# Kernel optimization log

Measured on AMD Instinct MI355X. Metric: run time of the kernel, lower is better.

## Reference

```python
import jax, jax.numpy as jnp
import numpy as np

B, L, D = 1, 4096, 1024
H, HD = 16, 64

def setup_inputs() -> dict:
    key = jax.random.key(0)
    ks = jax.random.split(key, 5)
    scale = 1.0 / np.sqrt(D)
    return {
        "x": jax.random.normal(ks[0], (B, L, D), dtype=jnp.float32),
        "Wq": jax.random.normal(ks[1], (D, D), dtype=jnp.float32) * scale,
        "Wk": jax.random.normal(ks[2], (D, D), dtype=jnp.float32) * scale,
        "Wv": jax.random.normal(ks[3], (D, D), dtype=jnp.float32) * scale,
        "Wo": jax.random.normal(ks[4], (D, D), dtype=jnp.float32) * scale,
    }

def reference(x, Wq, Wk, Wv, Wo):
    Bc, Lc, _ = x.shape
    # torch Linear: y = x @ W.T
    q = (x @ Wq.T).reshape(Bc, Lc, H, HD).transpose(0, 2, 1, 3)  # [B,H,L,hd]
    k = (x @ Wk.T).reshape(Bc, Lc, H, HD).transpose(0, 2, 1, 3)
    v = (x @ Wv.T).reshape(Bc, Lc, H, HD).transpose(0, 2, 1, 3)
    scale = HD ** -0.5
    scores = jnp.einsum('bhqd,bhkd->bhqk', q, k) * scale  # [B,H,L,L]
    causal = jnp.tril(jnp.ones((Lc, Lc), dtype=bool))
    scores = jnp.where(causal, scores, -jnp.inf)
    attn = jax.nn.softmax(scores, axis=-1)
    out = jnp.einsum('bhqk,bhkd->bhqd', attn, v)
    out = out.transpose(0, 2, 1, 3).reshape(Bc, Lc, H * HD)
    return out @ Wo.T
```

## Files before the change

### kernel.cpp

```cpp
#include <hip/hip_runtime.h>
#include <hip/hip_bf16.h>
#include <stdint.h>

#define L_SEQ   4096
#define D_MODEL 1024
#define N_HEADS 16
#define HEAD_DIM 64

typedef uint16_t u16;
typedef __bf16 bf16x8 __attribute__((ext_vector_type(8)));
typedef short s16x4 __attribute__((ext_vector_type(4)));
typedef float floatx4 __attribute__((ext_vector_type(4)));

__device__ __forceinline__ floatx4 mfma32(bf16x8 a, bf16x8 b, floatx4 c) {
  return __builtin_amdgcn_mfma_f32_16x16x32_bf16(a, b, c, 0, 0, 0);
}

__device__ __forceinline__ float hw_exp2(float x) {
  return __builtin_amdgcn_exp2f(x);
}

__device__ __forceinline__ uint32_t fbits(float f) {
  union { float f; uint32_t u; } x; x.f = f; return x.u;
}

__device__ __forceinline__ uint32_t pack_bf16_trunc(float f1, float f0) {
  return __builtin_amdgcn_perm(fbits(f1), fbits(f0), 0x07060302u);
}

__device__ __forceinline__ void load16_lds(const u16* g, u16* l) {
  __builtin_amdgcn_global_load_lds(
      (const __attribute__((address_space(1))) void*)g,
      (__attribute__((address_space(3))) void*)l, 16, 0, 0);
}

__device__ __forceinline__ u16 f2bf(float f) {
  uint32_t u = fbits(f);
  uint32_t r = u + 0x7FFFu + ((u >> 16) & 1u);
  return (u16)(r >> 16);
}

#define Q_PRESCALE 0.18033688011112042f

__global__ __launch_bounds__(256) void cvt_kernel(
    const float* __restrict__ x,  const float* __restrict__ wq,
    const float* __restrict__ wk, const float* __restrict__ wv,
    const float* __restrict__ wo,
    u16* __restrict__ xb, u16* __restrict__ wqb, u16* __restrict__ wkb,
    u16* __restrict__ wvb, u16* __restrict__ wob) {
  const int z = blockIdx.z;
  const float* s; u16* d; int n;
  if (z == 0)      { s = x;  d = xb;  n = L_SEQ * D_MODEL; }
  else if (z == 1) { s = wq; d = wqb; n = D_MODEL * D_MODEL; }
  else if (z == 2) { s = wk; d = wkb; n = D_MODEL * D_MODEL; }
  else if (z == 3) { s = wv; d = wvb; n = D_MODEL * D_MODEL; }
  else             { s = wo; d = wob; n = D_MODEL * D_MODEL; }
  const int stride = gridDim.x * 256 * 4;
  for (int i = (blockIdx.x * 256 + threadIdx.x) * 4; i < n; i += stride) {
    float4 v = *(const float4*)(s + i);
    ushort4 o;
    o.x = f2bf(v.x); o.y = f2bf(v.y); o.z = f2bf(v.z); o.w = f2bf(v.w);
    *(ushort4*)(d + i) = o;
  }
}

__global__ __launch_bounds__(256) void qkv_gemm_kernel(
    const u16* __restrict__ X,
    const u16* __restrict__ Wq, const u16* __restrict__ Wk, const u16* __restrict__ Wv,
    u16* __restrict__ Qo, u16* __restrict__ Ko, u16* __restrict__ VTo) {
  constexpr int BK = 32, Kdim = D_MODEL, NIT = Kdim / BK;
  __shared__ __align__(16) u16 As[2][128 * BK];
  __shared__ __align__(16) u16 Bs[2][128 * BK];

  const int b = blockIdx.x;
  const int g = b & 7, i2 = b >> 3;
  const int z = i2 % 3, j = i2 / 3;
  const int x = (g & 3) * 8 + (j & 7);
  const int y = (g >> 2) * 4 + (j >> 3);

  const u16* __restrict__ A;
  const u16* __restrict__ B;
  int m0, n0;
  if (z < 2) { A = X; B = z ? Wk : Wq; m0 = x * 128; n0 = y * 128; }
  else       { A = Wv; B = X;          m0 = y * 128; n0 = x * 128; }

  const int tid = threadIdx.x;
  const int wave = tid >> 6, lane = tid & 63;
  const int wm = wave & 1, wn = wave >> 1;
  const int quad = lane >> 4, l15 = lane & 15;

  floatx4 acc[4][4] = {};

  const int cbase = wave * 128;
  const int c0 = cbase + lane, c1 = c0 + 64;
  const int r0 = c0 >> 2, cc0 = (c0 & 3) * 8;
  const int r1 = c1 >> 2, cc1 = (c1 & 3) * 8;

  auto stage = [&](int k0, int sel) {
    load16_lds(&A[(size_t)(m0 + r0) * Kdim + k0 + cc0], &As[sel][cbase * 8]);
    load16_lds(&A[(size_t)(m0 + r1) * Kdim + k0 + cc1], &As[sel][(cbase + 64) * 8]);
    load16_lds(&B[(size_t)(n0 + r0) * Kdim + k0 + cc0], &Bs[sel][cbase * 8]);
    load16_lds(&B[(size_t)(n0 + r1) * Kdim + k0 + cc1], &Bs[sel][(cbase + 64) * 8]);
  };

  stage(0, 0);
  for (int kk = 0; kk < NIT; ++kk) {
    __syncthreads();
    if (kk + 1 < NIT) stage((kk + 1) * BK, (kk + 1) & 1);
    const u16* Asc = As[kk & 1];
    const u16* Bsc = Bs[kk & 1];

    bf16x8 af[4], wf[4];
#pragma unroll
    for (int i = 0; i < 4; ++i)
      af[i] = *(const bf16x8*)(&Asc[(wm * 64 + i * 16 + l15) * BK + quad * 8]);
#pragma unroll
    for (int jn = 0; jn < 4; ++jn)
      wf[jn] = *(const bf16x8*)(&Bsc[(wn * 64 + jn * 16 + l15) * BK + quad * 8]);
#pragma unroll
    for (int i = 0; i < 4; ++i)
#pragma unroll
      for (int jn = 0; jn < 4; ++jn)
        acc[i][jn] = mfma32(af[i], wf[jn], acc[i][jn]);
  }

  const float scale = (z == 0) ? Q_PRESCALE : 1.0f;
  u16* __restrict__ C = (z == 0) ? Qo : (z == 1) ? Ko : VTo;
#pragma unroll
  for (int i = 0; i < 4; ++i) {
    const int mb = m0 + wm * 64 + i * 16 + quad * 4;
#pragma unroll
    for (int jn = 0; jn < 4; ++jn) {
      const int n = n0 + wn * 64 + jn * 16 + l15;
#pragma unroll
      for (int r = 0; r < 4; ++r) {
        const int m = mb + r;
        if (z < 2) {
          C[(size_t)(n >> 6) * (size_t)L_SEQ * HEAD_DIM + (size_t)m * HEAD_DIM + (n & 63)] =
              f2bf(acc[i][jn][r] * scale);
        } else {
          C[(size_t)(m >> 6) * (size_t)L_SEQ * HEAD_DIM + (size_t)(m & 63) * L_SEQ + n] =
              f2bf(acc[i][jn][r]);
        }
      }
    }
  }
}

__global__ __launch_bounds__(256) void out_gemm_kernel(
    const u16* __restrict__ A, const u16* __restrict__ W, float* __restrict__ C) {
  constexpr int BK = 32, Kdim = D_MODEL, NIT = Kdim / BK;
  __shared__ __align__(16) u16 As[2][128 * BK];
  __shared__ __align__(16) u16 Bs[2][64 * BK];

  const int tid = threadIdx.x;
  const int wave = tid >> 6, lane = tid & 63;
  const int wm = wave & 1, wn = wave >> 1;
  const int quad = lane >> 4, l15 = lane & 15;
  const int m0 = blockIdx.x * 128, n0 = blockIdx.y * 64;

  floatx4 acc[4][2] = {};

  const int cbase = wave * 128;
  const int c0 = cbase + lane, c1 = c0 + 64;
  const int ra0 = c0 >> 2, ca0 = (c0 & 3) * 8;
  const int ra1 = c1 >> 2, ca1 = (c1 & 3) * 8;
  const int cb = wave * 64 + lane;
  const int rb = cb >> 2, cbcol = (cb & 3) * 8;

  auto stage = [&](int k0, int sel) {
    load16_lds(&A[(size_t)(m0 + ra0) * Kdim + k0 + ca0], &As[sel][cbase * 8]);
    load16_lds(&A[(size_t)(m0 + ra1) * Kdim + k0 + ca1], &As[sel][(cbase + 64) * 8]);
    load16_lds(&W[(size_t)(n0 + rb) * Kdim + k0 + cbcol], &Bs[sel][wave * 64 * 8]);
  };

  stage(0, 0);
  for (int kk = 0; kk < NIT; ++kk) {
    __syncthreads();
    if (kk + 1 < NIT) stage((kk + 1) * BK, (kk + 1) & 1);
    const u16* Asc = As[kk & 1];
    const u16* Bsc = Bs[kk & 1];

    bf16x8 af[4], wf[2];
#pragma unroll
    for (int i = 0; i < 4; ++i)
      af[i] = *(const bf16x8*)(&Asc[(wm * 64 + i * 16 + l15) * BK + quad * 8]);
#pragma unroll
    for (int jn = 0; jn < 2; ++jn)
      wf[jn] = *(const bf16x8*)(&Bsc[(wn * 32 + jn * 16 + l15) * BK + quad * 8]);
#pragma unroll
    for (int i = 0; i < 4; ++i)
#pragma unroll
      for (int jn = 0; jn < 2; ++jn)
        acc[i][jn] = mfma32(af[i], wf[jn], acc[i][jn]);
  }

#pragma unroll
  for (int i = 0; i < 4; ++i) {
    const int mb = m0 + wm * 64 + i * 16 + quad * 4;
#pragma unroll
    for (int jn = 0; jn < 2; ++jn) {
      const int n = n0 + wn * 32 + jn * 16 + l15;
#pragma unroll
      for (int r = 0; r < 4; ++r)
        C[(size_t)(mb + r) * D_MODEL + n] = acc[i][jn][r];
    }
  }
}

__global__ __launch_bounds__(256, 3) void attn_kernel(
    const u16* __restrict__ Q, const u16* __restrict__ K,
    const u16* __restrict__ VT, u16* __restrict__ Oa) {
  __shared__ __align__(16) union SMem {
    u16 V[4][4][64 * 16];
    float Of[4 * 64 * 16];
  } sm;
  __shared__ float Lf[4 * 64 + 64];

  const int b = blockIdx.x;
  const int h = b & 15;
  const int qt = 63 - (b >> 4);
  const int tid = threadIdx.x;
  const int wave = tid >> 6, lane = tid & 63;
  const int quad = lane >> 4, l15 = lane & 15;

  const size_t hoff = (size_t)h * L_SEQ * HEAD_DIM;
  const u16* __restrict__ Qh = Q + hoff;
  const u16* __restrict__ Kh = K + hoff;
  const u16* __restrict__ VTh = VT + hoff;

  const int q0 = qt * 64;
  const int np = (qt + 2) >> 1;

  const u16* const Kg = Kh + (size_t)(wave * 16 + l15) * HEAD_DIM;
  const u16* const Vsrc =
      VTh + (size_t)(lane >> 1) * L_SEQ + wave * 16 + (lane & 1) * 8;
  u16* const Vdst = &sm.V[0][0][0] + wave * 1024;

  bf16x8 qf[4][2];
#pragma unroll
  for (int jq = 0; jq < 4; ++jq) {
    const u16* qrow = Qh + (size_t)(q0 + jq * 16 + l15) * HEAD_DIM;
    qf[jq][0] = *(const bf16x8*)(qrow + quad * 8);
    qf[jq][1] = *(const bf16x8*)(qrow + 32 + quad * 8);
  }

  floatx4 oacc[4][4] = {};
  float psum[4] = {};

  load16_lds(Vsrc,                           Vdst);
  load16_lds(Vsrc + (size_t)32 * L_SEQ,      Vdst + 512);
  load16_lds(Vsrc + 64,                      Vdst + 4096);
  load16_lds(Vsrc + 64 + (size_t)32 * L_SEQ, Vdst + 4096 + 512);
  bf16x8 k00 = *(const bf16x8*)(Kg + quad * 8);
  bf16x8 k01 = *(const bf16x8*)(Kg + 32 + quad * 8);
  bf16x8 k10 = *(const bf16x8*)(Kg + (size_t)64 * HEAD_DIM + quad * 8);
  bf16x8 k11 = *(const bf16x8*)(Kg + (size_t)64 * HEAD_DIM + 32 + quad * 8);

  union PB { uint32_t w[4]; bf16x8 v; };

  for (int pt = 0; pt < np; ++pt) {
    asm volatile("s_waitcnt vmcnt(4)" ::: "memory");

    const u16* Va = &sm.V[(pt & 1) * 2][wave][0];
    const u16* Vb = Va + 4096;
    PB vf[4];
#pragma unroll
    for (int nt = 0; nt < 4; ++nt) {
      const int o = nt * 256 + l15 * 16 + quad * 4;
      uint2 lo = *(const uint2*)(Va + o);
      uint2 hi = *(const uint2*)(Vb + o);
      vf[nt].w[0] = lo.x; vf[nt].w[1] = lo.y;
      vf[nt].w[2] = hi.x; vf[nt].w[3] = hi.y;
    }

    if (pt + 1 < np) {
      const u16* src = Vsrc + (size_t)(pt + 1) * 128;
      u16* dst = Vdst + ((pt + 1) & 1) * 2 * 4096;
      load16_lds(src,                           dst);
      load16_lds(src + (size_t)32 * L_SEQ,      dst + 512);
      load16_lds(src + 64,                      dst + 4096);
      load16_lds(src + 64 + (size_t)32 * L_SEQ, dst + 4096 + 512);
    }

    const bool lastp = (pt == np - 1);
    const int kb = pt * 128 + wave * 16 + quad * 4;

#pragma unroll
    for (int jq = 0; jq < 4; ++jq) {
      floatx4 s0 = {}, s1 = {};
      s0 = mfma32(k00, qf[jq][0], s0);
      s0 = mfma32(k01, qf[jq][1], s0);
      s1 = mfma32(k10, qf[jq][0], s1);
      s1 = mfma32(k11, qf[jq][1], s1);

      if (lastp) {
        const int qg = q0 + jq * 16 + l15;
#pragma unroll
        for (int r = 0; r < 4; ++r) {
          if (kb + r > qg)      s0[r] = -1e30f;
          if (kb + 64 + r > qg) s1[r] = -1e30f;
        }
      }

      float p0 = hw_exp2(s0[0]), p1 = hw_exp2(s0[1]);
      float p2 = hw_exp2(s0[2]), p3 = hw_exp2(s0[3]);
      float r0 = hw_exp2(s1[0]), r1 = hw_exp2(s1[1]);
      float r2 = hw_exp2(s1[2]), r3 = hw_exp2(s1[3]);
      psum[jq] += ((p0 + p1) + (p2 + p3)) + ((r0 + r1) + (r2 + r3));

      PB pa;
      pa.w[0] = pack_bf16_trunc(p1, p0);
      pa.w[1] = pack_bf16_trunc(p3, p2);
      pa.w[2] = pack_bf16_trunc(r1, r0);
      pa.w[3] = pack_bf16_trunc(r3, r2);

#pragma unroll
      for (int nt = 0; nt < 4; ++nt)
        oacc[jq][nt] = mfma32(pa.v, vf[nt].v, oacc[jq][nt]);
    }

    if (pt + 1 < np) {
      asm volatile("" ::: "memory");
      const u16* kp = Kg + (size_t)(pt + 1) * 128 * HEAD_DIM;
      k00 = *(const bf16x8*)(kp + quad * 8);
      k01 = *(const bf16x8*)(kp + 32 + quad * 8);
      k10 = *(const bf16x8*)(kp + (size_t)64 * HEAD_DIM + quad * 8);
      k11 = *(const bf16x8*)(kp + (size_t)64 * HEAD_DIM + 32 + quad * 8);
    }
  }

#pragma unroll
  for (int jq = 0; jq < 4; ++jq) {
    psum[jq] += __shfl_xor(psum[jq], 16, 64);
    psum[jq] += __shfl_xor(psum[jq], 32, 64);
  }
  if (quad == 0) {
#pragma unroll
    for (int jq = 0; jq < 4; ++jq)
      Lf[wave * 64 + jq * 16 + l15] = psum[jq];
  }
  __syncthreads();
  if (tid < 64) {
    float lt = Lf[tid] + Lf[64 + tid] + Lf[128 + tid] + Lf[192 + tid];
    Lf[256 + tid] = 1.0f / lt;
  }

  const int qc = tid >> 2, d4 = (tid & 3) * 4;
#pragma unroll
  for (int nt = 0; nt < 4; ++nt) {
#pragma unroll
    for (int jq = 0; jq < 4; ++jq)
#pragma unroll
      for (int r = 0; r < 4; ++r)
        sm.Of[wave * 1024 + (jq * 16 + quad * 4 + r) * 16 + l15] = oacc[jq][nt][r];
    __syncthreads();
    const float invq = Lf[256 + qc];
    floatx4 a0 = *(const floatx4*)&sm.Of[0 * 1024 + qc * 16 + d4];
    floatx4 a1 = *(const floatx4*)&sm.Of[1 * 1024 + qc * 16 + d4];
    floatx4 a2 = *(const floatx4*)&sm.Of[2 * 1024 + qc * 16 + d4];
    floatx4 a3 = *(const floatx4*)&sm.Of[3 * 1024 + qc * 16 + d4];
    floatx4 sum = (a0 + a1) + (a2 + a3);
    ushort4 o;
    o.x = f2bf(sum[0] * invq); o.y = f2bf(sum[1] * invq);
    o.z = f2bf(sum[2] * invq); o.w = f2bf(sum[3] * invq);
    *(ushort4*)(Oa + (size_t)(q0 + qc) * D_MODEL + (size_t)h * HEAD_DIM +
                nt * 16 + d4) = o;
    __syncthreads();
  }
}

extern "C" void kernel_launch(void* const* d_in, const int* in_sizes, int n_in,
                              void* d_out, int out_size, void* d_ws, size_t ws_size,
                              hipStream_t stream) {
  const float* x  = (const float*)d_in[0];
  const float* Wq = (const float*)d_in[1];
  const float* Wk = (const float*)d_in[2];
  const float* Wv = (const float*)d_in[3];
  const float* Wo = (const float*)d_in[4];
  float* out = (float*)d_out;

  const size_t XN = (size_t)L_SEQ * D_MODEL;
  const size_t WN = (size_t)D_MODEL * D_MODEL;
  const size_t HLHD = (size_t)N_HEADS * L_SEQ * HEAD_DIM;

  u16* x_bf  = (u16*)d_ws;
  u16* wq_bf = x_bf + XN;
  u16* wk_bf = wq_bf + WN;
  u16* wv_bf = wk_bf + WN;
  u16* wo_bf = wv_bf + WN;
  u16* q_ws  = wo_bf + WN;
  u16* k_ws  = q_ws + HLHD;
  u16* vT_ws = k_ws + HLHD;
  u16* a_ws  = vT_ws + HLHD;

  dim3 gc(1024, 1, 5);
  cvt_kernel<<<gc, 256, 0, stream>>>(x, Wq, Wk, Wv, Wo,
                                     x_bf, wq_bf, wk_bf, wv_bf, wo_bf);

  dim3 gqkv(768, 1, 1);
  qkv_gemm_kernel<<<gqkv, 256, 0, stream>>>(x_bf, wq_bf, wk_bf, wv_bf,
                                            q_ws, k_ws, vT_ws);

  dim3 ga(1024, 1, 1);
  attn_kernel<<<ga, 256, 0, stream>>>(q_ws, k_ws, vT_ws, a_ws);

  dim3 go(L_SEQ / 128, D_MODEL / 64, 1);
  out_gemm_kernel<<<go, 256, 0, stream>>>(a_ws, wo_bf, out);
}
```

Baseline: 226.5 us.

## Stage V through registers into padded LDS and batch QK^T MFMAs before softmax

Replaces the direct global-to-LDS V loads with register-staged loads written into a padded shared tile (row stride 136), prefetched two tiles ahead. All QK^T MFMAs for a tile are issued first, then the next K fragment is loaded, then masking and exp are applied in a separate pass. The aim is to hide global latency and reduce LDS bank conflicts. The cost is more registers, and launch bounds drop from 3 to 2 waves per SIMD, which lowers occupancy. Each wave writes and reads only its own column slice of the shared V tile, which is presumably why no barrier was added.

```diff
diff --git a/kernel.cpp b/kernel.cpp
--- a/kernel.cpp
+++ b/kernel.cpp
@@ -9,7 +9,7 @@
 
 typedef uint16_t u16;
 typedef __bf16 bf16x8 __attribute__((ext_vector_type(8)));
-typedef short s16x4 __attribute__((ext_vector_type(4)));
+typedef uint32_t u32x4 __attribute__((ext_vector_type(4)));
 typedef float floatx4 __attribute__((ext_vector_type(4)));
 
 __device__ __forceinline__ floatx4 mfma32(bf16x8 a, bf16x8 b, floatx4 c) {
@@ -208,11 +208,12 @@
   }
 }
 
-__global__ __launch_bounds__(256, 3) void attn_kernel(
+#define LDW 136
+__global__ __launch_bounds__(256, 2) void attn_kernel(
     const u16* __restrict__ Q, const u16* __restrict__ K,
     const u16* __restrict__ VT, u16* __restrict__ Oa) {
   __shared__ __align__(16) union SMem {
-    u16 V[4][4][64 * 16];
+    u16 Vts[2][64 * LDW];
     float Of[4 * 64 * 16];
   } sm;
   __shared__ float Lf[4 * 64 + 64];
@@ -233,9 +234,15 @@
   const int np = (qt + 2) >> 1;
 
   const u16* const Kg = Kh + (size_t)(wave * 16 + l15) * HEAD_DIM;
-  const u16* const Vsrc =
-      VTh + (size_t)(lane >> 1) * L_SEQ + wave * 16 + (lane & 1) * 8;
-  u16* const Vdst = &sm.V[0][0][0] + wave * 1024;
+
+  const int vd0 = lane >> 1;
+  const int vk  = (lane & 1) * 8;
+  const int we0 = vd0 * LDW + wave * 16 + vk;
+  const int we1 = (vd0 + 32) * LDW + wave * 16 + vk;
+  const int wo0 = we0 + 64;
+  const int wo1 = we1 + 64;
+  const u16* const Vg0 = VTh + (size_t)vd0 * L_SEQ + wave * 16 + vk;
+  const u16* const Vg1 = Vg0 + (size_t)32 * L_SEQ;
 
   bf16x8 qf[4][2];
 #pragma unroll
@@ -248,85 +255,104 @@
   floatx4 oacc[4][4] = {};
   float psum[4] = {};
 
-  load16_lds(Vsrc,                           Vdst);
-  load16_lds(Vsrc + (size_t)32 * L_SEQ,      Vdst + 512);
-  load16_lds(Vsrc + 64,                      Vdst + 4096);
-  load16_lds(Vsrc + 64 + (size_t)32 * L_SEQ, Vdst + 4096 + 512);
-  bf16x8 k00 = *(const bf16x8*)(Kg + quad * 8);
-  bf16x8 k01 = *(const bf16x8*)(Kg + 32 + quad * 8);
-  bf16x8 k10 = *(const bf16x8*)(Kg + (size_t)64 * HEAD_DIM + quad * 8);
-  bf16x8 k11 = *(const bf16x8*)(Kg + (size_t)64 * HEAD_DIM + 32 + quad * 8);
-
-  union PB { uint32_t w[4]; bf16x8 v; };
+  float4 se0 = *(const float4*)(Vg0);
+  float4 se1 = *(const float4*)(Vg1);
+  float4 so0 = *(const float4*)(Vg0 + 64);
+  float4 so1 = *(const float4*)(Vg1 + 64);
+  *(float4*)(&sm.Vts[0][we0]) = se0;
+  *(float4*)(&sm.Vts[0][we1]) = se1;
+  *(float4*)(&sm.Vts[0][wo0]) = so0;
+  *(float4*)(&sm.Vts[0][wo1]) = so1;
+  if (np > 1) {
+    se0 = *(const float4*)(Vg0 + 128);
+    se1 = *(const float4*)(Vg1 + 128);
+    so0 = *(const float4*)(Vg0 + 192);
+    so1 = *(const float4*)(Vg1 + 192);
+  }
+  bf16x8 kc00 = *(const bf16x8*)(Kg + quad * 8);
+  bf16x8 kc01 = *(const bf16x8*)(Kg + 32 + quad * 8);
+  bf16x8 kc10 = *(const bf16x8*)(Kg + (size_t)64 * HEAD_DIM + quad * 8);
+  bf16x8 kc11 = *(const bf16x8*)(Kg + (size_t)64 * HEAD_DIM + 32 + quad * 8);
 
   for (int pt = 0; pt < np; ++pt) {
-    asm volatile("s_waitcnt vmcnt(4)" ::: "memory");
-
-    const u16* Va = &sm.V[(pt & 1) * 2][wave][0];
-    const u16* Vb = Va + 4096;
-    PB vf[4];
+    const u16* Vc = sm.Vts[pt & 1];
+    bf16x8 vf[4];
 #pragma unroll
     for (int nt = 0; nt < 4; ++nt) {
-      const int o = nt * 256 + l15 * 16 + quad * 4;
-      uint2 lo = *(const uint2*)(Va + o);
-      uint2 hi = *(const uint2*)(Vb + o);
-      vf[nt].w[0] = lo.x; vf[nt].w[1] = lo.y;
-      vf[nt].w[2] = hi.x; vf[nt].w[3] = hi.y;
+      const int rowb = (nt * 16 + l15) * LDW + wave * 16 + quad * 4;
+      uint2 lo = *(const uint2*)(&Vc[rowb]);
+      uint2 hi = *(const uint2*)(&Vc[rowb + 64]);
+      u32x4 t;
+      t.x = lo.x; t.y = lo.y; t.z = hi.x; t.w = hi.y;
+      vf[nt] = __builtin_bit_cast(bf16x8, t);
     }
 
     if (pt + 1 < np) {
-      const u16* src = Vsrc + (size_t)(pt + 1) * 128;
-      u16* dst = Vdst + ((pt + 1) & 1) * 2 * 4096;
-      load16_lds(src,                           dst);
-      load16_lds(src + (size_t)32 * L_SEQ,      dst + 512);
-      load16_lds(src + 64,                      dst + 4096);
-      load16_lds(src + 64 + (size_t)32 * L_SEQ, dst + 4096 + 512);
-    }
-
-    const bool lastp = (pt == np - 1);
-    const int kb = pt * 128 + wave * 16 + quad * 4;
-
+      u16* Vn = sm.Vts[(pt + 1) & 1];
+      *(float4*)(&Vn[we0]) = se0;
+      *(float4*)(&Vn[we1]) = se1;
+      *(float4*)(&Vn[wo0]) = so0;
+      *(float4*)(&Vn[wo1]) = so1;
+      if (pt + 2 < np) {
+        const u16* src0 = Vg0 + (size_t)(pt + 2) * 128;
+        const u16* src1 = Vg1 + (size_t)(pt + 2) * 128;
+        se0 = *(const float4*)(src0);
+        se1 = *(const float4*)(src1);
+        so0 = *(const float4*)(src0 + 64);
+        so1 = *(const float4*)(src1 + 64);
+      }
+    }
+
+    floatx4 s0[4], s1[4];
 #pragma unroll
     for (int jq = 0; jq < 4; ++jq) {
-      floatx4 s0 = {}, s1 = {};
-      s0 = mfma32(k00, qf[jq][0], s0);
-      s0 = mfma32(k01, qf[jq][1], s0);
-      s1 = mfma32(k10, qf[jq][0], s1);
-      s1 = mfma32(k11, qf[jq][1], s1);
-
-      if (lastp) {
+      floatx4 z = {};
+      z = mfma32(kc00, qf[jq][0], z);
+      z = mfma32(kc01, qf[jq][1], z);
+      s0[jq] = z;
+      floatx4 y = {};
+      y = mfma32(kc10, qf[jq][0], y);
+      y = mfma32(kc11, qf[jq][1], y);
+      s1[jq] = y;
+    }
+
+    if (pt + 1 < np) {
+      const u16* Kn = Kg + (size_t)(pt + 1) * 128 * HEAD_DIM;
+      kc00 = *(const bf16x8*)(Kn + quad * 8);
+      kc01 = *(const bf16x8*)(Kn + 32 + quad * 8);
+      kc10 = *(const bf16x8*)(Kn + (size_t)64 * HEAD_DIM + quad * 8);
+      kc11 = *(const bf16x8*)(Kn + (size_t)64 * HEAD_DIM + 32 + quad * 8);
+    }
+
+    if (pt == np - 1) {
+      const int kbe = pt * 128 + wave * 16 + quad * 4;
+#pragma unroll
+      for (int jq = 0; jq < 4; ++jq) {
         const int qg = q0 + jq * 16 + l15;
 #pragma unroll
         for (int r = 0; r < 4; ++r) {
-          if (kb + r > qg)      s0[r] = -1e30f;
-          if (kb + 64 + r > qg) s1[r] = -1e30f;
+          if (kbe + r > qg)      s0[jq][r] = -1e30f;
+          if (kbe + 64 + r > qg) s1[jq][r] = -1e30f;
         }
       }
-
-      float p0 = hw_exp2(s0[0]), p1 = hw_exp2(s0[1]);
-      float p2 = hw_exp2(s0[2]), p3 = hw_exp2(s0[3]);
-      float r0 = hw_exp2(s1[0]), r1 = hw_exp2(s1[1]);
-      float r2 = hw_exp2(s1[2]), r3 = hw_exp2(s1[3]);
+    }
+
+#pragma unroll
+    for (int jq = 0; jq < 4; ++jq) {
+      float p0 = hw_exp2(s0[jq][0]), p1 = hw_exp2(s0[jq][1]);
+      float p2 = hw_exp2(s0[jq][2]), p3 = hw_exp2(s0[jq][3]);
+      float r0 = hw_exp2(s1[jq][0]), r1 = hw_exp2(s1[jq][1]);
+      float r2 = hw_exp2(s1[jq][2]), r3 = hw_exp2(s1[jq][3]);
       psum[jq] += ((p0 + p1) + (p2 + p3)) + ((r0 + r1) + (r2 + r3));
-
-      PB pa;
-      pa.w[0] = pack_bf16_trunc(p1, p0);
-      pa.w[1] = pack_bf16_trunc(p3, p2);
-      pa.w[2] = pack_bf16_trunc(r1, r0);
-      pa.w[3] = pack_bf16_trunc(r3, r2);
-
+      u32x4 pw;
+      pw.x = pack_bf16_trunc(p1, p0);
+      pw.y = pack_bf16_trunc(p3, p2);
+      pw.z = pack_bf16_trunc(r1, r0);
+      pw.w = pack_bf16_trunc(r3, r2);
+      bf16x8 pav = __builtin_bit_cast(bf16x8, pw);
 #pragma unroll
       for (int nt = 0; nt < 4; ++nt)
-        oacc[jq][nt] = mfma32(pa.v, vf[nt].v, oacc[jq][nt]);
-    }
-
-    if (pt + 1 < np) {
-      asm volatile("" ::: "memory");
-      const u16* kp = Kg + (size_t)(pt + 1) * 128 * HEAD_DIM;
-      k00 = *(const bf16x8*)(kp + quad * 8);
-      k01 = *(const bf16x8*)(kp + 32 + quad * 8);
-      k10 = *(const bf16x8*)(kp + (size_t)64 * HEAD_DIM + quad * 8);
-      k11 = *(const bf16x8*)(kp + (size_t)64 * HEAD_DIM + 32 + quad * 8);
+        oacc[jq][nt] = mfma32(pav, vf[nt], oacc[jq][nt]);
     }
   }
 
```

Measured after the change: 197.7 us. 12.7% less time.
